# Kernel tuning notes

Measured on AMD Instinct MI355X. Metric: run time of the kernel, lower is better.

## Reference

```python
import jax, jax.numpy as jnp
import numpy as np
from jax import lax

N_SAMPLES = 2 ** 15          # 32768
N_FRAMES = 128
N_HARMONICS = 8
FILT_SIZE = 64
N_EVENTS = 8
N_SCALE = 128                # len(MusicalScale()) assumed = 128 (MIDI notes)
NYQ = 11025.0                # SR22050 nyquist
MIN_F0 = 40.0 / NYQ
MAX_F0 = 3000.0 / NYQ
F0_SPAN = MAX_F0 - MIN_F0
MIN_RES = 0.9
RES_SPAN = 1.0 - MIN_RES
PI = float(np.pi)

# packed layout slices (order of param_sizes dict)
SL_F0 = slice(0, 128)
SL_FINE = slice(128, 256)
SL_AMP = slice(256, 384)
SL_HAMP = slice(384, 392)
SL_HDEC = slice(392, 400)
SL_FENV = slice(400, 464)


def lin_interp(x, out_size):
    """F.interpolate(mode='linear', align_corners=False) along last axis."""
    n = x.shape[-1]
    pos = (jnp.arange(out_size, dtype=x.dtype) + 0.5) * (n / out_size) - 0.5
    pos = jnp.clip(pos, 0.0, n - 1)
    lo = jnp.floor(pos).astype(jnp.int32)
    hi = jnp.minimum(lo + 1, n - 1)
    w = pos - lo.astype(x.dtype)
    return x[..., lo] * (1.0 - w) + x[..., hi] * w


def setup_inputs() -> dict:
    key = jax.random.key(0)
    k1, k2 = jax.random.split(key)
    B = 32 * N_EVENTS  # 256 event rows
    packed = jax.random.normal(k1, (B, 464), dtype=jnp.float32)
    # musical scale: MIDI-note center frequencies normalized by nyquist
    midi = np.arange(N_SCALE)
    freqs = 440.0 * 2.0 ** ((midi - 69) / 12.0) / NYQ
    frequencies = jnp.asarray(freqs, dtype=jnp.float32)
    noise = jax.random.uniform(k2, (B, 1, N_SAMPLES), dtype=jnp.float32)  # mapped to (-1,1) in reference
    return {"packed": packed, "frequencies": frequencies, "noise": noise}


def reference(packed, frequencies, noise):
    B = packed.shape[0]
    p = jax.nn.sigmoid(packed)  # Model applies activation(p) before SynthParams

    # f0: softmax over discrete scale bins, weighted sum of normalized freqs
    f0w = jax.nn.softmax(p[:, SL_F0], axis=-1)             # [B, 128]
    f0 = (f0w @ frequencies)[:, None, None]                # [B,1,1]
    f0 = jnp.broadcast_to(f0, (B, 1, N_FRAMES))            # repeat over frames
    f0 = f0 * NYQ
    f0 = MIN_F0 + f0 * F0_SPAN                             # [B,1,128]
    # NOTE: source computes `f0 + f0 + f0_fine` and discards it -> f0_fine unused

    harmonic_factors = jnp.arange(1, N_HARMONICS + 1, dtype=p.dtype)
    osc = f0 * harmonic_factors[None, :, None]             # [B,8,128]
    radians = osc / NYQ * PI
    radians = lin_interp(radians, N_SAMPLES)               # [B,8,32768]
    osc_bank = jnp.sin(jnp.cumsum(radians, axis=-1))

    harm_decay = MIN_RES + p[:, SL_HDEC] * RES_SPAN        # [B,8]
    harm_amp = p[:, SL_HAMP]                               # [B,8]
    amp = p[:, SL_AMP][:, None, :] * 2.0 - 1.0             # [B,1,128]
    amp_full = lin_interp(amp, N_SAMPLES)                  # [B,1,32768]

    noise_filter = p[:, SL_FENV][:, None, :]               # [B,1,64]
    noise_filter = lin_interp(noise_filter, N_SAMPLES // 2)
    noise_filter = jnp.pad(noise_filter, ((0, 0), (0, 0), (0, 1)))  # [B,1,16385]

    noise_u = noise * 2.0 - 1.0                            # uniform(-1,1)
    noise_spec = jnp.fft.rfft(noise_u, axis=-1, norm='ortho')
    filt = jnp.fft.irfft(noise_spec * noise_filter, n=N_SAMPLES, axis=-1, norm='ortho')
    filt = filt * jnp.clip(amp_full, 0.0, 1.0)             # [B,1,32768]

    # leaky-accumulator recurrence over frames
    def step(cur, a_i):  # cur [B,8], a_i [B]
        cur = jnp.clip(cur + a_i[:, None] * harm_amp, 0.0, 1.0)
        out = cur
        cur = cur * harm_decay
        return cur, out

    amp_t = amp[:, 0, :].T                                 # [128, B]
    _, outs = lax.scan(step, jnp.zeros((B, N_HARMONICS), dtype=p.dtype), amp_t)
    x = jnp.transpose(outs, (1, 2, 0))                     # [B,8,128]
    x = jnp.where(x >= PI, 0.0, x)
    x = lin_interp(x, N_SAMPLES)                           # [B,8,32768]
    x = x * osc_bank
    x = filt + x
    x = x.reshape(-1, N_EVENTS, N_HARMONICS, N_SAMPLES)
    x = jnp.sum(x, axis=(1, 2))[:, None, :]                # [batch,1,32768]
    return x
```

## Files before the change

kernel.cpp:

```cpp
#include <hip/hip_runtime.h>
#include <math.h>

#ifndef M_PI
#define M_PI 3.14159265358979323846
#endif

#define NSAMP 32768
#define MHALF 16384
#define TWO_PI_F 6.2831853071795864f
#define PSTRIDE 1089

typedef float v2 __attribute__((ext_vector_type(2)));

__device__ __forceinline__ double dsig(double x) { return 1.0 / (1.0 + exp(-x)); }

__device__ __forceinline__ v2 cmul(v2 a, v2 b) {
    return a.xx * b + (v2){-a.y, a.y} * b.yx;
}

template<int INV>
__device__ __forceinline__ void fft4(v2& x0, v2& x1, v2& x2, v2& x3) {
    v2 s02 = x0 + x2;
    v2 d02 = x0 - x2;
    v2 s13 = x1 + x3;
    v2 d13 = x1 - x3;
    v2 j13 = INV ? (v2){-d13.y, d13.x} : (v2){d13.y, -d13.x};
    x0 = s02 + s13;
    x2 = s02 - s13;
    x1 = d02 + j13;
    x3 = d02 - j13;
}

#define V16(v, c) v[((((c) & 3) << 2) | ((c) >> 2))]

template<int INV>
__device__ __forceinline__ void fft16(v2 v[16]) {
    const float s = INV ? 1.0f : -1.0f;
#pragma unroll
    for (int b = 0; b < 4; b++) fft4<INV>(v[b], v[4 + b], v[8 + b], v[12 + b]);
    v[5]  = cmul(v[5],  (v2){0.9238795325f,  s * 0.3826834324f});
    v[9]  = cmul(v[9],  (v2){0.7071067812f,  s * 0.7071067812f});
    v[13] = cmul(v[13], (v2){0.3826834324f,  s * 0.9238795325f});
    v[6]  = cmul(v[6],  (v2){0.7071067812f,  s * 0.7071067812f});
    v[10] = cmul(v[10], (v2){0.0f,           s * 1.0f});
    v[14] = cmul(v[14], (v2){-0.7071067812f, s * 0.7071067812f});
    v[7]  = cmul(v[7],  (v2){0.3826834324f,  s * 0.9238795325f});
    v[11] = cmul(v[11], (v2){-0.7071067812f, s * 0.7071067812f});
    v[15] = cmul(v[15], (v2){-0.9238795325f, s * -0.3826834324f});
#pragma unroll
    for (int p = 0; p < 4; p++) fft4<INV>(v[4 * p], v[4 * p + 1], v[4 * p + 2], v[4 * p + 3]);
}

__device__ __forceinline__ int zaddr(int k) {
    int p = k & 15, k2 = k >> 4;
    int s = 256 * (k2 & 3) + 16 * ((k2 >> 2) & 15) + (k2 >> 6);
    return p * PSTRIDE + s + (s >> 4);
}

__device__ __forceinline__ void plane_fwd(v2* __restrict__ Zp, int l) {
    {
        float sn, cs;
        __sincosf(TWO_PI_F * (float)l * (1.f / 1024.f), &sn, &cs);
        v2 w1 = (v2){cs, -sn};
        const v2 jstep = (v2){0.9238795325f, -0.3826834324f};
#pragma unroll
        for (int j = 0; j < 4; j++) {
            const int r = 64 * j + l;
            v2 u0 = Zp[r], u1 = Zp[256 + r], u2 = Zp[512 + r], u3 = Zp[768 + r];
            fft4<0>(u0, u1, u2, u3);
            v2 w2 = cmul(w1, w1);
            v2 w3 = cmul(w2, w1);
            Zp[r] = u0;
            Zp[256 + r] = cmul(u1, w1);
            Zp[512 + r] = cmul(u2, w2);
            Zp[768 + r] = cmul(u3, w3);
            w1 = cmul(w1, jstep);
        }
    }
    {
        const int k4 = l >> 4, c = l & 15;
        const int nbase = 256 * k4 + c;
        float sn, cs;
        __sincosf(TWO_PI_F * (float)c * (1.f / 256.f), &sn, &cs);
        const v2 wc = (v2){cs, -sn};
        v2 v[16];
#pragma unroll
        for (int b = 0; b < 16; b++) v[b] = Zp[nbase + 16 * b];
        fft16<0>(v);
        const int pbase = 272 * k4 + c;
        Zp[pbase] = V16(v, 0);
        v2 w = wc;
#pragma unroll
        for (int kb = 1; kb < 16; kb++) {
            Zp[pbase + 17 * kb] = cmul(V16(v, kb), w);
            w = cmul(w, wc);
        }
    }
    {
        const int pbase = 272 * (l >> 4) + 17 * (l & 15);
        v2 v[16];
#pragma unroll
        for (int c = 0; c < 16; c++) v[c] = Zp[pbase + c];
        fft16<0>(v);
#pragma unroll
        for (int kc = 0; kc < 16; kc++) Zp[pbase + kc] = V16(v, kc);
    }
}

__device__ __forceinline__ void plane_inv(v2* __restrict__ Zp, int l) {
    {
        const int kb = l & 15;
        const int pbase = 272 * (l >> 4) + 17 * kb;
        float sn, cs;
        __sincosf(TWO_PI_F * (float)kb * (1.f / 256.f), &sn, &cs);
        const v2 wkb = (v2){cs, sn};
        v2 v[16];
#pragma unroll
        for (int kc = 0; kc < 16; kc++) v[kc] = Zp[pbase + kc];
        fft16<1>(v);
        Zp[pbase] = V16(v, 0);
        v2 w = wkb;
#pragma unroll
        for (int nc = 1; nc < 16; nc++) {
            Zp[pbase + nc] = cmul(V16(v, nc), w);
            w = cmul(w, wkb);
        }
    }
    {
        const int k4 = l >> 4, nc = l & 15;
        const int pbase = 272 * k4 + nc;
        float sni, csi;
        __sincosf(TWO_PI_F * (float)(nc * k4) * (1.f / 1024.f), &sni, &csi);
        v2 t = (v2){csi, sni};
        float sns, css;
        __sincosf(TWO_PI_F * (float)k4 * (1.f / 64.f), &sns, &css);
        const v2 st = (v2){css, sns};
        v2 v[16];
#pragma unroll
        for (int kb = 0; kb < 16; kb++) v[kb] = Zp[pbase + 17 * kb];
        fft16<1>(v);
#pragma unroll
        for (int nb = 0; nb < 16; nb++) {
            Zp[pbase + 17 * nb] = cmul(V16(v, nb), t);
            t = cmul(t, st);
        }
    }
#pragma unroll
    for (int j = 0; j < 4; j++) {
        const int r = 64 * j + l;
        const int rp = r + (r >> 4);
        v2 u0 = Zp[rp], u1 = Zp[272 + rp], u2 = Zp[544 + rp], u3 = Zp[816 + rp];
        fft4<1>(u0, u1, u2, u3);
        Zp[rp] = u0; Zp[272 + rp] = u1; Zp[544 + rp] = u2; Zp[816 + rp] = u3;
    }
}

__device__ __forceinline__ float hinterp64(const float* f, int j) {
    float pos = ((float)j + 0.5f) * (1.0f / 256.0f) - 0.5f;
    pos = fminf(fmaxf(pos, 0.0f), 63.0f);
    int lo = (int)pos;
    int hi = min(lo + 1, 63);
    float w = pos - (float)lo;
    return f[lo] * (1.0f - w) + f[hi] * w;
}

template<int J>
__device__ __forceinline__ void synth_chunk(
    int tid, const float* __restrict__ env_s,
    const unsigned long long* __restrict__ step_s, float* __restrict__ po)
{
    const int s0 = (tid << 2) + (J << 12);

    float c0v[4], c1v[4], c2v[4];
    float pos0 = ((float)s0 + 0.5f) * (1.0f / 256.0f) - 0.5f;
    pos0 = fminf(fmaxf(pos0, 0.0f), 127.0f);
    const int lo0 = (int)pos0;
#pragma unroll
    for (int k = 0; k < 4; k++) {
        float pos = ((float)(s0 + k) + 0.5f) * (1.0f / 256.0f) - 0.5f;
        pos = fminf(fmaxf(pos, 0.0f), 127.0f);
        int lo = (int)pos;
        float w = pos - (float)lo;
        if (lo == lo0) { c0v[k] = 1.0f - w; c1v[k] = w;        c2v[k] = 0.0f; }
        else           { c0v[k] = 0.0f;     c1v[k] = 1.0f - w; c2v[k] = w;    }
    }
    const int i1 = min(lo0 + 1, 127);
    float pos3 = ((float)(s0 + 3) + 0.5f) * (1.0f / 256.0f) - 0.5f;
    pos3 = fminf(fmaxf(pos3, 0.0f), 127.0f);
    const int i2 = min((int)pos3 + 1, 127);

    float v0a[8], v1a[8], v2a[8];
#pragma unroll
    for (int h = 0; h < 8; h++) {
        const float* er = env_s + (h << 7);
        v0a[h] = er[lo0]; v1a[h] = er[i1]; v2a[h] = er[i2];
    }

    const unsigned long long st1 = step_s[0];
    const float stf1 = (float)(unsigned)(st1 >> 32) * 0x1p-32f;
    const unsigned long long pp = st1 * (unsigned long long)(unsigned)(s0 + 1);
    float fr = (float)(unsigned)(pp >> 32) * 0x1p-32f;

    float out[4];
#pragma unroll
    for (int k = 0; k < 4; k++) {
        const float sn = __builtin_amdgcn_sinf(fr);
        const float cs = __builtin_amdgcn_cosf(fr);
        const float c2 = cs + cs;
        float s_prev = 0.0f, s_cur = sn;
        float a = 0.0f;
#pragma unroll
        for (int h = 0; h < 8; h++) {
            const float ev = fmaf(v0a[h], c0v[k], fmaf(v1a[h], c1v[k], v2a[h] * c2v[k]));
            a = fmaf(ev, s_cur, a);
            const float s_next = fmaf(c2, s_cur, -s_prev);
            s_prev = s_cur; s_cur = s_next;
        }
        out[k] = a;
        fr = __builtin_amdgcn_fractf(fr + stf1);
    }
    *(float4*)(po + s0) = make_float4(out[0], out[1], out[2], out[3]);
}

__global__ __launch_bounds__(1024)
__attribute__((amdgpu_waves_per_eu(4, 4)))
void fused_kernel(
    const float* __restrict__ packed, const float* __restrict__ freqs,
    const float* __restrict__ noise, float* __restrict__ part)
{
    __shared__ v2 Z[16 * PSTRIDE];
    __shared__ float fenv_s[64];
    __shared__ float amp_s[128];
    __shared__ float env_s[8 * 128];
    __shared__ unsigned long long step_s[8];

    const int bid = blockIdx.x;
    const int g = (bid & 7) + 8 * ((bid >> 3) & 3);
    const int bb = g * 8 + (bid >> 5);
    const int tid = threadIdx.x;
    const int wv = tid >> 6, l = tid & 63;

    float* po_sine = part + ((size_t)(256 + bb) << 15);

    if (tid < 64) {
        const float* pk = packed + bb * 464;
        double e0 = exp(dsig((double)pk[tid]));
        double e1 = exp(dsig((double)pk[tid + 64]));
        double num = e0 * (double)freqs[tid] + e1 * (double)freqs[tid + 64];
        double den = e0 + e1;
#pragma unroll
        for (int off = 32; off > 0; off >>= 1) {
            num += __shfl_down(num, off);
            den += __shfl_down(den, off);
        }
        num = __shfl(num, 0);
        den = __shfl(den, 0);

        float a0 = (float)(dsig((double)pk[256 + tid]) * 2.0 - 1.0);
        float a1 = (float)(dsig((double)pk[256 + 64 + tid]) * 2.0 - 1.0);
        amp_s[tid] = a0; amp_s[tid + 64] = a1;
        fenv_s[tid] = (float)dsig((double)pk[400 + tid]);

        if (tid < 8) {
            const double NYQ = 11025.0;
            const double MIN_F0 = 40.0 / NYQ;
            const double MAX_F0 = 3000.0 / NYQ;
            const double F0_SPAN = MAX_F0 - MIN_F0;
            double f0 = num / den;
            double F = f0 * NYQ;
            double G = MIN_F0 + F * F0_SPAN;
            double oscf = G * (double)(tid + 1);
            double r = oscf / NYQ * M_PI;
            double rv = r / (2.0 * M_PI);
            rv -= floor(rv);
            step_s[tid] = (unsigned long long)(rv * 18446744073709551616.0);

            float ha = (float)dsig((double)pk[384 + tid]);
            float hd = 0.9f + (float)dsig((double)pk[392 + tid]) * 0.1f;
            float cur = 0.0f;
            float* eo = env_s + (tid << 7);
            for (int fr = 0; fr < 128; fr++) {
                cur = fmaf(amp_s[fr], ha, cur);
                cur = fminf(fmaxf(cur, 0.0f), 1.0f);
                eo[fr] = cur;
                cur *= hd;
            }
        }
    }

    const v2* nz = (const v2*)(noise + (size_t)bb * NSAMP);

    {
        v2 v[16];
#pragma unroll
        for (int a = 0; a < 16; a++) {
            v2 t = nz[a * 1024 + tid];
            v[a] = t * 2.f - 1.f;
        }
        fft16<0>(v);
        float sn, cs;
        __sincosf(TWO_PI_F * (float)tid * (1.f / 16384.f), &sn, &cs);
        const v2 ws = (v2){cs, -sn};
        Z[tid] = V16(v, 0);
        v2 w = ws;
#pragma unroll
        for (int k1 = 1; k1 < 16; k1++) {
            Z[k1 * PSTRIDE + tid] = cmul(V16(v, k1), w);
            w = cmul(w, ws);
        }
    }
    __syncthreads();

    synth_chunk<0>(tid, env_s, step_s, po_sine);
    synth_chunk<1>(tid, env_s, step_s, po_sine);

    plane_fwd(Z + wv * PSTRIDE, l);

    synth_chunk<2>(tid, env_s, step_s, po_sine);
    synth_chunk<3>(tid, env_s, step_s, po_sine);
    __syncthreads();

    const float invM = 1.0f / (float)MHALF;
    {
        float sn0, cs0;
        __sincosf((float)M_PI * (float)tid * (1.f / 16384.f), &sn0, &cs0);
        v2 t = (v2){cs0, sn0};
        const v2 tstep = (v2){0.98078528040323f, 0.19509032201613f};
        for (int k = tid; k <= 8192; k += 1024) {
            if (k == 0) {
                int i0 = zaddr(0);
                v2 Z0 = Z[i0];
                float Y0 = (Z0.x + Z0.y) * hinterp64(fenv_s, 0);
                float vv = Y0 * 0.5f * invM;
                Z[i0] = (v2){vv, vv};
            } else if (k == 8192) {
                int i8 = zaddr(8192);
                float s = hinterp64(fenv_s, 8192) * invM;
                Z[i8] = Z[i8] * s;
            } else {
                int ik = zaddr(k), imk = zaddr(16384 - k);
                v2 Zk = Z[ik], Zm = Z[imk];
                float Ex = 0.5f * (Zk.x + Zm.x);
                float Ey = 0.5f * (Zk.y - Zm.y);
                float Ox = 0.5f * (Zk.y + Zm.y);
                float Oy = -0.5f * (Zk.x - Zm.x);
                float cs = t.x, sn = t.y;
                float Xkx = Ex + cs * Ox + sn * Oy;
                float Xky = Ey + cs * Oy - sn * Ox;
                float Xmx = Ex - cs * Ox - sn * Oy;
                float Xmy = -Ey + cs * Oy - sn * Ox;
                float Hk = hinterp64(fenv_s, k);
                float Hm = hinterp64(fenv_s, 16384 - k);
                float Ykx = Xkx * Hk, Yky = Xky * Hk;
                float Ymx = Xmx * Hm, Ymy = Xmy * Hm;
                float Er = 0.5f * (Ykx + Ymx);
                float Ei = 0.5f * (Yky - Ymy);
                float Pr = 0.5f * (Ykx - Ymx);
                float Pi = 0.5f * (Yky + Ymy);
                float Oyx = Pr * cs - Pi * sn;
                float Oyy = Pr * sn + Pi * cs;
                Z[ik]  = (v2){(Er - Oyy) * invM, (Ei + Oyx) * invM};
                Z[imk] = (v2){(Er + Oyy) * invM, (-Ei + Oyx) * invM};
            }
            t = cmul(t, tstep);
        }
    }

    synth_chunk<4>(tid, env_s, step_s, po_sine);
    synth_chunk<5>(tid, env_s, step_s, po_sine);
    __syncthreads();

    plane_inv(Z + wv * PSTRIDE, l);

    synth_chunk<6>(tid, env_s, step_s, po_sine);
    synth_chunk<7>(tid, env_s, step_s, po_sine);
    __syncthreads();

    {
        const int tp = tid + (tid >> 4);
        v2 v[16];
#pragma unroll
        for (int k1 = 0; k1 < 16; k1++) v[k1] = Z[k1 * PSTRIDE + tp];
        float sn, cs;
        __sincosf(TWO_PI_F * (float)tid * (1.f / 16384.f), &sn, &cs);
        const v2 wg = (v2){cs, sn};
        v2 w = wg;
#pragma unroll
        for (int k1 = 1; k1 < 16; k1++) {
            v[k1] = cmul(v[k1], w);
            w = cmul(w, wg);
        }
        fft16<1>(v);

        v2* fo = (v2*)(part + ((size_t)bb << 15));
#pragma unroll
        for (int m = 0; m < 16; m++) {
            v2 y = V16(v, m);
            int A = m * 1024 + tid;
            int s0 = 2 * A;
            float p0 = ((float)s0 + 0.5f) * (1.0f / 256.0f) - 0.5f;
            float p1 = p0 + (1.0f / 256.0f);
            p0 = fminf(fmaxf(p0, 0.0f), 127.0f);
            p1 = fminf(fmaxf(p1, 0.0f), 127.0f);
            int l0 = (int)p0, l1 = (int)p1;
            int h0 = min(l0 + 1, 127), h1 = min(l1 + 1, 127);
            float w0a = p0 - (float)l0, w1a = p1 - (float)l1;
            float a0 = amp_s[l0] * (1.0f - w0a) + amp_s[h0] * w0a;
            float a1 = amp_s[l1] * (1.0f - w1a) + amp_s[h1] * w1a;
            a0 = fminf(fmaxf(a0, 0.0f), 1.0f);
            a1 = fminf(fmaxf(a1, 0.0f), 1.0f);
            fo[A] = (v2){8.0f * y.x * a0, 8.0f * y.y * a1};
        }
    }
}

__global__ __launch_bounds__(256) void reduce_kernel(
    const float* __restrict__ part, float* __restrict__ out)
{
    const int b = blockIdx.x;
    const int g = (b & 7) + 8 * ((b >> 3) & 3);
    const int chunk = b >> 5;
    const int s = (chunk << 10) + ((int)threadIdx.x << 2);

    float4 a = make_float4(0.f, 0.f, 0.f, 0.f);
#pragma unroll
    for (int e = 0; e < 8; e++) {
        const float4 f  = *(const float4*)(part + ((size_t)(g * 8 + e) << 15) + s);
        const float4 sn = *(const float4*)(part + ((size_t)(256 + g * 8 + e) << 15) + s);
        a.x += f.x + sn.x; a.y += f.y + sn.y;
        a.z += f.z + sn.z; a.w += f.w + sn.w;
    }
    *(float4*)(out + ((size_t)g << 15) + s) = a;
}

extern "C" void kernel_launch(void* const* d_in, const int* in_sizes, int n_in,
                              void* d_out, int out_size, void* d_ws, size_t ws_size,
                              hipStream_t stream)
{
    (void)in_sizes; (void)n_in; (void)out_size; (void)ws_size;
    const float* packed = (const float*)d_in[0];
    const float* freqs  = (const float*)d_in[1];
    const float* noise  = (const float*)d_in[2];
    float* out = (float*)d_out;
    float* part = (float*)d_ws;

    hipLaunchKernelGGL(fused_kernel, dim3(256), dim3(1024), 0, stream,
                       packed, freqs, noise, part);
    hipLaunchKernelGGL(reduce_kernel, dim3(1024), dim3(256), 0, stream,
                       part, out);
}
```

Baseline: 120.2 us.

## Fuse reduction into cooperative kernel and synthesize sines after grid sync

Replaces the two-kernel scheme with one cooperative launch. Each block writes its envelope and step data to workspace. After a grid-wide sync, each block builds the sine-bank contribution of all 8 events for its output chunk and adds the filtered-noise partials directly into the output. This drops the per-event sine partial buffers (256x32768 floats written and read back) and the second launch. In exchange it adds a grid sync and loses the overlap of synthesis with the FFT phases. It also relies on all 256 blocks of 1024 threads being co-resident.

```diff
diff --git a/kernel.cpp b/kernel.cpp
--- a/kernel.cpp
+++ b/kernel.cpp
@@ -1,5 +1,8 @@
 #include <hip/hip_runtime.h>
+#include <hip/hip_cooperative_groups.h>
 #include <math.h>
+
+namespace cg = cooperative_groups;
 
 #ifndef M_PI
 #define M_PI 3.14159265358979323846
@@ -164,83 +167,27 @@
     return f[lo] * (1.0f - w) + f[hi] * w;
 }
 
-template<int J>
-__device__ __forceinline__ void synth_chunk(
-    int tid, const float* __restrict__ env_s,
-    const unsigned long long* __restrict__ step_s, float* __restrict__ po)
-{
-    const int s0 = (tid << 2) + (J << 12);
-
-    float c0v[4], c1v[4], c2v[4];
-    float pos0 = ((float)s0 + 0.5f) * (1.0f / 256.0f) - 0.5f;
-    pos0 = fminf(fmaxf(pos0, 0.0f), 127.0f);
-    const int lo0 = (int)pos0;
-#pragma unroll
-    for (int k = 0; k < 4; k++) {
-        float pos = ((float)(s0 + k) + 0.5f) * (1.0f / 256.0f) - 0.5f;
-        pos = fminf(fmaxf(pos, 0.0f), 127.0f);
-        int lo = (int)pos;
-        float w = pos - (float)lo;
-        if (lo == lo0) { c0v[k] = 1.0f - w; c1v[k] = w;        c2v[k] = 0.0f; }
-        else           { c0v[k] = 0.0f;     c1v[k] = 1.0f - w; c2v[k] = w;    }
-    }
-    const int i1 = min(lo0 + 1, 127);
-    float pos3 = ((float)(s0 + 3) + 0.5f) * (1.0f / 256.0f) - 0.5f;
-    pos3 = fminf(fmaxf(pos3, 0.0f), 127.0f);
-    const int i2 = min((int)pos3 + 1, 127);
-
-    float v0a[8], v1a[8], v2a[8];
-#pragma unroll
-    for (int h = 0; h < 8; h++) {
-        const float* er = env_s + (h << 7);
-        v0a[h] = er[lo0]; v1a[h] = er[i1]; v2a[h] = er[i2];
-    }
-
-    const unsigned long long st1 = step_s[0];
-    const float stf1 = (float)(unsigned)(st1 >> 32) * 0x1p-32f;
-    const unsigned long long pp = st1 * (unsigned long long)(unsigned)(s0 + 1);
-    float fr = (float)(unsigned)(pp >> 32) * 0x1p-32f;
-
-    float out[4];
-#pragma unroll
-    for (int k = 0; k < 4; k++) {
-        const float sn = __builtin_amdgcn_sinf(fr);
-        const float cs = __builtin_amdgcn_cosf(fr);
-        const float c2 = cs + cs;
-        float s_prev = 0.0f, s_cur = sn;
-        float a = 0.0f;
-#pragma unroll
-        for (int h = 0; h < 8; h++) {
-            const float ev = fmaf(v0a[h], c0v[k], fmaf(v1a[h], c1v[k], v2a[h] * c2v[k]));
-            a = fmaf(ev, s_cur, a);
-            const float s_next = fmaf(c2, s_cur, -s_prev);
-            s_prev = s_cur; s_cur = s_next;
-        }
-        out[k] = a;
-        fr = __builtin_amdgcn_fractf(fr + stf1);
-    }
-    *(float4*)(po + s0) = make_float4(out[0], out[1], out[2], out[3]);
-}
-
 __global__ __launch_bounds__(1024)
 __attribute__((amdgpu_waves_per_eu(4, 4)))
 void fused_kernel(
     const float* __restrict__ packed, const float* __restrict__ freqs,
-    const float* __restrict__ noise, float* __restrict__ part)
+    const float* __restrict__ noise, float* __restrict__ part,
+    float* __restrict__ env_ws, unsigned long long* __restrict__ step_ws,
+    float* __restrict__ out)
 {
     __shared__ v2 Z[16 * PSTRIDE];
     __shared__ float fenv_s[64];
     __shared__ float amp_s[128];
     __shared__ float env_s[8 * 128];
     __shared__ unsigned long long step_s[8];
+    __shared__ unsigned long long stepg[8];
 
     const int bid = blockIdx.x;
     const int g = (bid & 7) + 8 * ((bid >> 3) & 3);
-    const int bb = g * 8 + (bid >> 5);
+    const int echunk = bid >> 5;
+    const int bb = g * 8 + echunk;
     const int tid = threadIdx.x;
     const int wv = tid >> 6, l = tid & 63;
-
-    float* po_sine = part + ((size_t)(256 + bb) << 15);
 
     if (tid < 64) {
         const float* pk = packed + bb * 464;
@@ -311,13 +258,10 @@
     }
     __syncthreads();
 
-    synth_chunk<0>(tid, env_s, step_s, po_sine);
-    synth_chunk<1>(tid, env_s, step_s, po_sine);
+    env_ws[((size_t)bb << 10) + tid] = env_s[tid];
+    if (tid < 8) step_ws[((size_t)bb << 3) + tid] = step_s[tid];
 
     plane_fwd(Z + wv * PSTRIDE, l);
-
-    synth_chunk<2>(tid, env_s, step_s, po_sine);
-    synth_chunk<3>(tid, env_s, step_s, po_sine);
     __syncthreads();
 
     const float invM = 1.0f / (float)MHALF;
@@ -365,15 +309,9 @@
             t = cmul(t, tstep);
         }
     }
-
-    synth_chunk<4>(tid, env_s, step_s, po_sine);
-    synth_chunk<5>(tid, env_s, step_s, po_sine);
     __syncthreads();
 
     plane_inv(Z + wv * PSTRIDE, l);
-
-    synth_chunk<6>(tid, env_s, step_s, po_sine);
-    synth_chunk<7>(tid, env_s, step_s, po_sine);
     __syncthreads();
 
     {
@@ -412,25 +350,81 @@
             fo[A] = (v2){8.0f * y.x * a0, 8.0f * y.y * a1};
         }
     }
-}
-
-__global__ __launch_bounds__(256) void reduce_kernel(
-    const float* __restrict__ part, float* __restrict__ out)
-{
-    const int b = blockIdx.x;
-    const int g = (b & 7) + 8 * ((b >> 3) & 3);
-    const int chunk = b >> 5;
-    const int s = (chunk << 10) + ((int)threadIdx.x << 2);
-
-    float4 a = make_float4(0.f, 0.f, 0.f, 0.f);
-#pragma unroll
-    for (int e = 0; e < 8; e++) {
-        const float4 f  = *(const float4*)(part + ((size_t)(g * 8 + e) << 15) + s);
-        const float4 sn = *(const float4*)(part + ((size_t)(256 + g * 8 + e) << 15) + s);
-        a.x += f.x + sn.x; a.y += f.y + sn.y;
-        a.z += f.z + sn.z; a.w += f.w + sn.w;
-    }
-    *(float4*)(out + ((size_t)g << 15) + s) = a;
+
+    cg::this_grid().sync();
+
+    {
+        float* env2 = (float*)Z;
+        const float* eg = env_ws + ((size_t)g << 13);
+#pragma unroll
+        for (int i = 0; i < 8; i++) env2[(i << 10) + tid] = eg[(i << 10) + tid];
+        if (tid < 8) stepg[tid] = step_ws[(size_t)((g << 3) + tid) << 3];
+        __syncthreads();
+
+        const int s0 = (echunk << 12) + (tid << 2);
+
+        float c0v[4], c1v[4], c2v[4];
+        float pos0 = ((float)s0 + 0.5f) * (1.0f / 256.0f) - 0.5f;
+        pos0 = fminf(fmaxf(pos0, 0.0f), 127.0f);
+        const int lo0 = (int)pos0;
+#pragma unroll
+        for (int k = 0; k < 4; k++) {
+            float pos = ((float)(s0 + k) + 0.5f) * (1.0f / 256.0f) - 0.5f;
+            pos = fminf(fmaxf(pos, 0.0f), 127.0f);
+            int lo = (int)pos;
+            float w = pos - (float)lo;
+            if (lo == lo0) { c0v[k] = 1.0f - w; c1v[k] = w;        c2v[k] = 0.0f; }
+            else           { c0v[k] = 0.0f;     c1v[k] = 1.0f - w; c2v[k] = w;    }
+        }
+        const int i1 = min(lo0 + 1, 127);
+        float pos3 = ((float)(s0 + 3) + 0.5f) * (1.0f / 256.0f) - 0.5f;
+        pos3 = fminf(fmaxf(pos3, 0.0f), 127.0f);
+        const int i2 = min((int)pos3 + 1, 127);
+
+        float a0 = 0.f, a1 = 0.f, a2 = 0.f, a3 = 0.f;
+#pragma unroll
+        for (int e = 0; e < 8; e++) {
+            const float4 f = *(const float4*)(part + ((size_t)((g << 3) + e) << 15) + s0);
+            a0 += f.x; a1 += f.y; a2 += f.z; a3 += f.w;
+        }
+
+#pragma unroll 1
+        for (int e = 0; e < 8; e++) {
+            const unsigned long long st1 = stepg[e];
+            const float stf1 = (float)(unsigned)(st1 >> 32) * 0x1p-32f;
+            const unsigned long long pp = st1 * (unsigned long long)(unsigned)(s0 + 1);
+            float fr = (float)(unsigned)(pp >> 32) * 0x1p-32f;
+
+            float v0a[8], v1a[8], v2a[8];
+            const float* er = env2 + (e << 10);
+#pragma unroll
+            for (int h = 0; h < 8; h++) {
+                v0a[h] = er[(h << 7) + lo0];
+                v1a[h] = er[(h << 7) + i1];
+                v2a[h] = er[(h << 7) + i2];
+            }
+            float s_out[4];
+#pragma unroll
+            for (int k = 0; k < 4; k++) {
+                const float sn = __builtin_amdgcn_sinf(fr);
+                const float cs = __builtin_amdgcn_cosf(fr);
+                const float c2 = cs + cs;
+                float s_prev = 0.0f, s_cur = sn, a = 0.0f;
+#pragma unroll
+                for (int h = 0; h < 8; h++) {
+                    const float ev = fmaf(v0a[h], c0v[k], fmaf(v1a[h], c1v[k], v2a[h] * c2v[k]));
+                    a = fmaf(ev, s_cur, a);
+                    const float s_next = fmaf(c2, s_cur, -s_prev);
+                    s_prev = s_cur; s_cur = s_next;
+                }
+                s_out[k] = a;
+                fr = __builtin_amdgcn_fractf(fr + stf1);
+            }
+            a0 += s_out[0]; a1 += s_out[1]; a2 += s_out[2]; a3 += s_out[3];
+        }
+
+        *(float4*)(out + ((size_t)g << 15) + s0) = make_float4(a0, a1, a2, a3);
+    }
 }
 
 extern "C" void kernel_launch(void* const* d_in, const int* in_sizes, int n_in,
@@ -442,10 +436,15 @@
     const float* freqs  = (const float*)d_in[1];
     const float* noise  = (const float*)d_in[2];
     float* out = (float*)d_out;
-    float* part = (float*)d_ws;
-
-    hipLaunchKernelGGL(fused_kernel, dim3(256), dim3(1024), 0, stream,
-                       packed, freqs, noise, part);
-    hipLaunchKernelGGL(reduce_kernel, dim3(1024), dim3(256), 0, stream,
-                       part, out);
-}
+    char* ws = (char*)d_ws;
+
+    float* part = (float*)ws;
+    float* env_ws = (float*)(ws + (size_t)32 * 1024 * 1024);
+    unsigned long long* step_ws =
+        (unsigned long long*)(ws + (size_t)33 * 1024 * 1024);
+
+    void* args[] = { (void*)&packed, (void*)&freqs, (void*)&noise,
+                     (void*)&part, (void*)&env_ws, (void*)&step_ws, (void*)&out };
+    hipLaunchCooperativeKernel((void*)fused_kernel, dim3(256), dim3(1024),
+                               args, 0, stream);
+}
```

Result: slower. 154.4 us (+28.5%).

## Split sine synthesis by sample chunk across events, accumulate in registers, skip per-event partials

Applied to the files above, without the earlier changes.

Each block now synthesizes the sine-bank contribution for one 4096-sample chunk across all 8 events of its group, instead of one full event. It accumulates the sum in registers and writes it straight to the output buffer, which removes the 256 per-event sine partial arrays and halves the reads in the reduce kernel. To support this, the first 8 waves each compute f0, step and a windowed envelope (18 frames) for one event, with the frame recurrence done per lane via shuffles. The cost is redundant parameter and envelope computation in every block and an extra read of the output buffer in the reduce kernel.

```diff
diff --git a/kernel.cpp b/kernel.cpp
--- a/kernel.cpp
+++ b/kernel.cpp
@@ -164,51 +164,34 @@
     return f[lo] * (1.0f - w) + f[hi] * w;
 }
 
-template<int J>
-__device__ __forceinline__ void synth_chunk(
-    int tid, const float* __restrict__ env_s,
-    const unsigned long long* __restrict__ step_s, float* __restrict__ po)
+__device__ __forceinline__ void synth_event(
+    int e, int s0, const float* __restrict__ envg,
+    const unsigned long long* __restrict__ stepg,
+    const float c0v[4], const float c1v[4], const float c2v[4],
+    int j0, int j1, int j2, float4& acc)
 {
-    const int s0 = (tid << 2) + (J << 12);
-
-    float c0v[4], c1v[4], c2v[4];
-    float pos0 = ((float)s0 + 0.5f) * (1.0f / 256.0f) - 0.5f;
-    pos0 = fminf(fmaxf(pos0, 0.0f), 127.0f);
-    const int lo0 = (int)pos0;
-#pragma unroll
-    for (int k = 0; k < 4; k++) {
-        float pos = ((float)(s0 + k) + 0.5f) * (1.0f / 256.0f) - 0.5f;
-        pos = fminf(fmaxf(pos, 0.0f), 127.0f);
-        int lo = (int)pos;
-        float w = pos - (float)lo;
-        if (lo == lo0) { c0v[k] = 1.0f - w; c1v[k] = w;        c2v[k] = 0.0f; }
-        else           { c0v[k] = 0.0f;     c1v[k] = 1.0f - w; c2v[k] = w;    }
-    }
-    const int i1 = min(lo0 + 1, 127);
-    float pos3 = ((float)(s0 + 3) + 0.5f) * (1.0f / 256.0f) - 0.5f;
-    pos3 = fminf(fmaxf(pos3, 0.0f), 127.0f);
-    const int i2 = min((int)pos3 + 1, 127);
-
-    float v0a[8], v1a[8], v2a[8];
-#pragma unroll
-    for (int h = 0; h < 8; h++) {
-        const float* er = env_s + (h << 7);
-        v0a[h] = er[lo0]; v1a[h] = er[i1]; v2a[h] = er[i2];
-    }
-
-    const unsigned long long st1 = step_s[0];
+    const unsigned long long st1 = stepg[e];
     const float stf1 = (float)(unsigned)(st1 >> 32) * 0x1p-32f;
     const unsigned long long pp = st1 * (unsigned long long)(unsigned)(s0 + 1);
     float fr = (float)(unsigned)(pp >> 32) * 0x1p-32f;
 
+    float v0a[8], v1a[8], v2a[8];
+    const float* er = envg + e * (8 * 18);
+#pragma unroll
+    for (int h = 0; h < 8; h++) {
+        v0a[h] = er[h * 18 + j0];
+        v1a[h] = er[h * 18 + j1];
+        v2a[h] = er[h * 18 + j2];
+    }
+
+    float a0 = acc.x, a1 = acc.y, a2 = acc.z, a3 = acc.w;
     float out[4];
 #pragma unroll
     for (int k = 0; k < 4; k++) {
         const float sn = __builtin_amdgcn_sinf(fr);
         const float cs = __builtin_amdgcn_cosf(fr);
         const float c2 = cs + cs;
-        float s_prev = 0.0f, s_cur = sn;
-        float a = 0.0f;
+        float s_prev = 0.0f, s_cur = sn, a = 0.0f;
 #pragma unroll
         for (int h = 0; h < 8; h++) {
             const float ev = fmaf(v0a[h], c0v[k], fmaf(v1a[h], c1v[k], v2a[h] * c2v[k]));
@@ -219,34 +202,35 @@
         out[k] = a;
         fr = __builtin_amdgcn_fractf(fr + stf1);
     }
-    *(float4*)(po + s0) = make_float4(out[0], out[1], out[2], out[3]);
+    acc = make_float4(a0 + out[0], a1 + out[1], a2 + out[2], a3 + out[3]);
 }
 
 __global__ __launch_bounds__(1024)
 __attribute__((amdgpu_waves_per_eu(4, 4)))
 void fused_kernel(
     const float* __restrict__ packed, const float* __restrict__ freqs,
-    const float* __restrict__ noise, float* __restrict__ part)
+    const float* __restrict__ noise, float* __restrict__ part,
+    float* __restrict__ out)
 {
     __shared__ v2 Z[16 * PSTRIDE];
     __shared__ float fenv_s[64];
     __shared__ float amp_s[128];
-    __shared__ float env_s[8 * 128];
-    __shared__ unsigned long long step_s[8];
+    __shared__ float envg[8][8][18];
+    __shared__ unsigned long long stepg[8];
 
     const int bid = blockIdx.x;
     const int g = (bid & 7) + 8 * ((bid >> 3) & 3);
-    const int bb = g * 8 + (bid >> 5);
+    const int echunk = bid >> 5;
+    const int bb = g * 8 + echunk;
     const int tid = threadIdx.x;
     const int wv = tid >> 6, l = tid & 63;
 
-    float* po_sine = part + ((size_t)(256 + bb) << 15);
-
-    if (tid < 64) {
-        const float* pk = packed + bb * 464;
-        double e0 = exp(dsig((double)pk[tid]));
-        double e1 = exp(dsig((double)pk[tid + 64]));
-        double num = e0 * (double)freqs[tid] + e1 * (double)freqs[tid + 64];
+    if (wv < 8) {
+        const int ev = g * 8 + wv;
+        const float* pk = packed + ev * 464;
+        double e0 = exp(dsig((double)pk[l]));
+        double e1 = exp(dsig((double)pk[l + 64]));
+        double num = e0 * (double)freqs[l] + e1 * (double)freqs[l + 64];
         double den = e0 + e1;
 #pragma unroll
         for (int off = 32; off > 0; off >>= 1) {
@@ -256,37 +240,64 @@
         num = __shfl(num, 0);
         den = __shfl(den, 0);
 
-        float a0 = (float)(dsig((double)pk[256 + tid]) * 2.0 - 1.0);
-        float a1 = (float)(dsig((double)pk[256 + 64 + tid]) * 2.0 - 1.0);
-        amp_s[tid] = a0; amp_s[tid + 64] = a1;
-        fenv_s[tid] = (float)dsig((double)pk[400 + tid]);
-
-        if (tid < 8) {
+        float a0 = (float)(dsig((double)pk[256 + l]) * 2.0 - 1.0);
+        float a1 = (float)(dsig((double)pk[256 + 64 + l]) * 2.0 - 1.0);
+        if (wv == echunk) {
+            amp_s[l] = a0; amp_s[l + 64] = a1;
+            fenv_s[l] = (float)dsig((double)pk[400 + l]);
+        }
+
+        if (l == 0) {
             const double NYQ = 11025.0;
             const double MIN_F0 = 40.0 / NYQ;
             const double MAX_F0 = 3000.0 / NYQ;
             const double F0_SPAN = MAX_F0 - MIN_F0;
             double f0 = num / den;
-            double F = f0 * NYQ;
-            double G = MIN_F0 + F * F0_SPAN;
-            double oscf = G * (double)(tid + 1);
-            double r = oscf / NYQ * M_PI;
+            double G = MIN_F0 + f0 * NYQ * F0_SPAN;
+            double r = G / NYQ * M_PI;
             double rv = r / (2.0 * M_PI);
             rv -= floor(rv);
-            step_s[tid] = (unsigned long long)(rv * 18446744073709551616.0);
-
-            float ha = (float)dsig((double)pk[384 + tid]);
-            float hd = 0.9f + (float)dsig((double)pk[392 + tid]) * 0.1f;
-            float cur = 0.0f;
-            float* eo = env_s + (tid << 7);
-            for (int fr = 0; fr < 128; fr++) {
-                cur = fmaf(amp_s[fr], ha, cur);
-                cur = fminf(fmaxf(cur, 0.0f), 1.0f);
-                eo[fr] = cur;
-                cur *= hd;
-            }
-        }
-    }
+            stepg[wv] = (unsigned long long)(rv * 18446744073709551616.0);
+        }
+
+        const int wbase = max(0, echunk * 16 - 1);
+        const int hh = l & 7;
+        float ha = (float)dsig((double)pk[384 + hh]);
+        float hd = 0.9f + (float)dsig((double)pk[392 + hh]) * 0.1f;
+        float cur = 0.0f;
+        for (int fr = 0; fr < 128; fr++) {
+            const float af = __shfl(fr < 64 ? a0 : a1, fr & 63);
+            cur = fmaf(af, ha, cur);
+            cur = fminf(fmaxf(cur, 0.0f), 1.0f);
+            if (l < 8 && fr >= wbase && fr < wbase + 18) envg[wv][l][fr - wbase] = cur;
+            cur *= hd;
+        }
+    }
+
+    const int s0c = (echunk << 12) + (tid << 2);
+    float c0v[4], c1v[4], c2v[4];
+    int j0, j1, j2;
+    {
+        float pos0 = ((float)s0c + 0.5f) * (1.0f / 256.0f) - 0.5f;
+        pos0 = fminf(fmaxf(pos0, 0.0f), 127.0f);
+        const int lo0 = (int)pos0;
+#pragma unroll
+        for (int k = 0; k < 4; k++) {
+            float pos = ((float)(s0c + k) + 0.5f) * (1.0f / 256.0f) - 0.5f;
+            pos = fminf(fmaxf(pos, 0.0f), 127.0f);
+            int lo = (int)pos;
+            float w = pos - (float)lo;
+            if (lo == lo0) { c0v[k] = 1.0f - w; c1v[k] = w;        c2v[k] = 0.0f; }
+            else           { c0v[k] = 0.0f;     c1v[k] = 1.0f - w; c2v[k] = w;    }
+        }
+        const int i1 = min(lo0 + 1, 127);
+        float pos3 = ((float)(s0c + 3) + 0.5f) * (1.0f / 256.0f) - 0.5f;
+        pos3 = fminf(fmaxf(pos3, 0.0f), 127.0f);
+        const int i2 = min((int)pos3 + 1, 127);
+        const int wbase = max(0, echunk * 16 - 1);
+        j0 = lo0 - wbase; j1 = i1 - wbase; j2 = i2 - wbase;
+    }
+    float4 acc = make_float4(0.f, 0.f, 0.f, 0.f);
 
     const v2* nz = (const v2*)(noise + (size_t)bb * NSAMP);
 
@@ -311,13 +322,13 @@
     }
     __syncthreads();
 
-    synth_chunk<0>(tid, env_s, step_s, po_sine);
-    synth_chunk<1>(tid, env_s, step_s, po_sine);
+    synth_event(0, s0c, &envg[0][0][0], stepg, c0v, c1v, c2v, j0, j1, j2, acc);
+    synth_event(1, s0c, &envg[0][0][0], stepg, c0v, c1v, c2v, j0, j1, j2, acc);
 
     plane_fwd(Z + wv * PSTRIDE, l);
 
-    synth_chunk<2>(tid, env_s, step_s, po_sine);
-    synth_chunk<3>(tid, env_s, step_s, po_sine);
+    synth_event(2, s0c, &envg[0][0][0], stepg, c0v, c1v, c2v, j0, j1, j2, acc);
+    synth_event(3, s0c, &envg[0][0][0], stepg, c0v, c1v, c2v, j0, j1, j2, acc);
     __syncthreads();
 
     const float invM = 1.0f / (float)MHALF;
@@ -366,14 +377,16 @@
         }
     }
 
-    synth_chunk<4>(tid, env_s, step_s, po_sine);
-    synth_chunk<5>(tid, env_s, step_s, po_sine);
+    synth_event(4, s0c, &envg[0][0][0], stepg, c0v, c1v, c2v, j0, j1, j2, acc);
+    synth_event(5, s0c, &envg[0][0][0], stepg, c0v, c1v, c2v, j0, j1, j2, acc);
     __syncthreads();
 
     plane_inv(Z + wv * PSTRIDE, l);
 
-    synth_chunk<6>(tid, env_s, step_s, po_sine);
-    synth_chunk<7>(tid, env_s, step_s, po_sine);
+    synth_event(6, s0c, &envg[0][0][0], stepg, c0v, c1v, c2v, j0, j1, j2, acc);
+    synth_event(7, s0c, &envg[0][0][0], stepg, c0v, c1v, c2v, j0, j1, j2, acc);
+
+    *(float4*)(out + ((size_t)g << 15) + s0c) = acc;
     __syncthreads();
 
     {
@@ -422,13 +435,11 @@
     const int chunk = b >> 5;
     const int s = (chunk << 10) + ((int)threadIdx.x << 2);
 
-    float4 a = make_float4(0.f, 0.f, 0.f, 0.f);
+    float4 a = *(const float4*)(out + ((size_t)g << 15) + s);
 #pragma unroll
     for (int e = 0; e < 8; e++) {
-        const float4 f  = *(const float4*)(part + ((size_t)(g * 8 + e) << 15) + s);
-        const float4 sn = *(const float4*)(part + ((size_t)(256 + g * 8 + e) << 15) + s);
-        a.x += f.x + sn.x; a.y += f.y + sn.y;
-        a.z += f.z + sn.z; a.w += f.w + sn.w;
+        const float4 f = *(const float4*)(part + ((size_t)(g * 8 + e) << 15) + s);
+        a.x += f.x; a.y += f.y; a.z += f.z; a.w += f.w;
     }
     *(float4*)(out + ((size_t)g << 15) + s) = a;
 }
@@ -445,7 +456,7 @@
     float* part = (float*)d_ws;
 
     hipLaunchKernelGGL(fused_kernel, dim3(256), dim3(1024), 0, stream,
-                       packed, freqs, noise, part);
+                       packed, freqs, noise, part, out);
     hipLaunchKernelGGL(reduce_kernel, dim3(1024), dim3(256), 0, stream,
                        part, out);
 }
```

New measurement: 313.2 us. 2.61x slower.
